# Kernel tuning notes

Measured on AMD Instinct MI355X. Metric: run time of the kernel, lower is better.

Reference implementation:

```python
import jax, jax.numpy as jnp
import numpy as np


def setup_inputs() -> dict:
    key = jax.random.key(0)
    ks = jax.random.split(key, 6)
    B, d, S = 256, 512, 196  # batch, hidden dim, spatial locations (14x14)
    return {
        "memory_state": jax.random.normal(ks[0], (B, d), dtype=jnp.float32),
        "ctrl_state": jax.random.normal(ks[1], (B, d), dtype=jnp.float32),
        "kb_proj": jax.random.normal(ks[2], (B, d, S), dtype=jnp.float32),
        "W_concat": jax.random.normal(ks[3], (d, d), dtype=jnp.float32) * (1.0 / np.sqrt(d)),
        "b_concat": jax.random.normal(ks[4], (d,), dtype=jnp.float32) * 0.01,
        "w_attn": jax.random.normal(ks[5], (d,), dtype=jnp.float32) * (1.0 / np.sqrt(d)),
    }


def reference(memory_state, ctrl_state, kb_proj, W_concat, b_concat, w_attn):
    # I_elements: [B, S, d] -- elementwise gating of knowledge base by memory
    I_t = memory_state[:, :, None] * kb_proj           # [B, d, S]
    I_t = jnp.transpose(I_t, (0, 2, 1))                # [B, S, d]
    # concat_layer (torch Linear: x @ W^T + b) + residual with kb_proj
    concat = jnp.einsum('bsd,ed->bse', I_t, W_concat) + b_concat
    concat = concat + jnp.transpose(kb_proj, (0, 2, 1))  # [B, S, d]
    # attention logits: (concat * ctrl) @ w_attn -> [B, S]
    rai = jnp.einsum('bsd,d->bs', concat * ctrl_state[:, None, :], w_attn)
    rvi = jax.nn.softmax(rai, axis=1)                  # [B, S]
    # attention-weighted sum over spatial locations -> [B, d]
    read_vector = jnp.einsum('bs,bds->bd', rvi, kb_proj)
    return read_vector
```

## Files before the change

### kernel.cpp

```cpp
#include <hip/hip_runtime.h>
#include <math.h>

#define B 256
#define D 512
#define S 196
#define SQ 49
#define NCH 8

__global__ __launch_bounds__(256) void k_gemm(const float* __restrict__ ctrl,
                                              const float* __restrict__ w_attn,
                                              const float* __restrict__ W,
                                              float* __restrict__ gpart) {
    __shared__ float u_s[64][8];
    const int ce = blockIdx.x >> 5;
    const int b0 = (blockIdx.x & 31) * 8;
    const int t = threadIdx.x;
#pragma unroll
    for (int k = t; k < 512; k += 256) {
        const int j = k & 7, el = k >> 3;
        const int e = ce * 64 + el;
        u_s[el][j] = ctrl[(b0 + j) * D + e] * w_attn[e];
    }
    __syncthreads();
    float a0[8], a1[8];
#pragma unroll
    for (int j = 0; j < 8; ++j) { a0[j] = 0.f; a1[j] = 0.f; }
    for (int e0 = 0; e0 < 64; e0 += 4) {
        float w0[4], w1[4];
#pragma unroll
        for (int i = 0; i < 4; ++i) {
            const int e = ce * 64 + e0 + i;
            w0[i] = W[e * D + t];
            w1[i] = W[e * D + t + 256];
        }
#pragma unroll
        for (int i = 0; i < 4; ++i) {
            const float4 ua = *(const float4*)&u_s[e0 + i][0];
            const float4 ub = *(const float4*)&u_s[e0 + i][4];
            a0[0] += ua.x * w0[i]; a0[1] += ua.y * w0[i];
            a0[2] += ua.z * w0[i]; a0[3] += ua.w * w0[i];
            a0[4] += ub.x * w0[i]; a0[5] += ub.y * w0[i];
            a0[6] += ub.z * w0[i]; a0[7] += ub.w * w0[i];
            a1[0] += ua.x * w1[i]; a1[1] += ua.y * w1[i];
            a1[2] += ua.z * w1[i]; a1[3] += ua.w * w1[i];
            a1[4] += ub.x * w1[i]; a1[5] += ub.y * w1[i];
            a1[6] += ub.z * w1[i]; a1[7] += ub.w * w1[i];
        }
    }
#pragma unroll
    for (int j = 0; j < 8; ++j) {
        gpart[((size_t)(b0 + j) * NCH + ce) * D + t]       = a0[j];
        gpart[((size_t)(b0 + j) * NCH + ce) * D + t + 256] = a1[j];
    }
}

__global__ __launch_bounds__(256) void k_logits(const float* __restrict__ kb,
                                                const float* __restrict__ gpart,
                                                const float* __restrict__ mem,
                                                const float* __restrict__ ctrl,
                                                const float* __restrict__ w_attn,
                                                float* __restrict__ rai_part) {
    __shared__ float p_s[64];
    __shared__ float part[4][S];
    const int bid = blockIdx.x;
    const int b = bid >> 3, c = bid & 7;
    const int t = threadIdx.x;
    const int w = t >> 6, l = t & 63;
    if (t < 64) {
        const int d = c * 64 + t;
        float s = 0.f;
#pragma unroll
        for (int ce = 0; ce < NCH; ++ce)
            s += gpart[((size_t)b * NCH + ce) * D + d];
        p_s[t] = mem[b * D + d] * s + ctrl[b * D + d] * w_attn[d];
    }
    __syncthreads();
    const float* base = kb + (size_t)b * D * S + (size_t)c * 64 * S;
    if (l < SQ) {
        float4 acc0 = {0.f, 0.f, 0.f, 0.f}, acc1 = {0.f, 0.f, 0.f, 0.f};
        for (int i = 0; i < 8; ++i) {
            const int r0 = w * 16 + i, r1 = w * 16 + 8 + i;
            const float4 v0 = *(const float4*)(base + (size_t)r0 * S + 4 * l);
            const float4 v1 = *(const float4*)(base + (size_t)r1 * S + 4 * l);
            const float pv0 = p_s[r0], pv1 = p_s[r1];
            acc0.x += pv0 * v0.x; acc0.y += pv0 * v0.y;
            acc0.z += pv0 * v0.z; acc0.w += pv0 * v0.w;
            acc1.x += pv1 * v1.x; acc1.y += pv1 * v1.y;
            acc1.z += pv1 * v1.z; acc1.w += pv1 * v1.w;
        }
        part[w][4 * l + 0] = acc0.x + acc1.x;
        part[w][4 * l + 1] = acc0.y + acc1.y;
        part[w][4 * l + 2] = acc0.z + acc1.z;
        part[w][4 * l + 3] = acc0.w + acc1.w;
    }
    __syncthreads();
    if (t < S)
        rai_part[(size_t)bid * S + t] = (part[0][t] + part[1][t]) + (part[2][t] + part[3][t]);
}

__global__ __launch_bounds__(256) void k_wsum(const float* __restrict__ kb,
                                              const float* __restrict__ rai_part,
                                              float* __restrict__ out) {
    __shared__ float rvi_s[S];
    __shared__ float redm[4], reds[4];
    const int bid = blockIdx.x;
    const int b = bid >> 3, c = bid & 7;
    const int t = threadIdx.x;
    const int w = t >> 6, l = t & 63;
    float rai = -INFINITY;
    if (t < S) {
        float v = 0.f;
#pragma unroll
        for (int k = 0; k < NCH; ++k)
            v += rai_part[((size_t)b * NCH + k) * S + t];
        rai = v;
    }
    float m = rai;
#pragma unroll
    for (int o = 1; o < 64; o <<= 1) m = fmaxf(m, __shfl_xor(m, o, 64));
    if (l == 0) redm[w] = m;
    __syncthreads();
    m = fmaxf(fmaxf(redm[0], redm[1]), fmaxf(redm[2], redm[3]));
    float ex = (t < S) ? __expf(rai - m) : 0.f;
    float sm = ex;
#pragma unroll
    for (int o = 1; o < 64; o <<= 1) sm += __shfl_xor(sm, o, 64);
    if (l == 0) reds[w] = sm;
    __syncthreads();
    const float li = (reds[0] + reds[1]) + (reds[2] + reds[3]);
    if (t < S) rvi_s[t] = ex / li;
    __syncthreads();

    float4 rv = {0.f, 0.f, 0.f, 0.f};
    if (l < SQ) rv = *(const float4*)&rvi_s[4 * l];
    const float* base = kb + (size_t)b * D * S + (size_t)c * 64 * S;
#pragma unroll
    for (int i = 0; i < 8; ++i) {
        const int r0 = w * 16 + i, r1 = w * 16 + 8 + i;
        float a0 = 0.f, a1 = 0.f;
        if (l < SQ) {
            const float4 v0 = *(const float4*)(base + (size_t)r0 * S + 4 * l);
            const float4 v1 = *(const float4*)(base + (size_t)r1 * S + 4 * l);
            a0 = rv.x * v0.x + rv.y * v0.y + rv.z * v0.z + rv.w * v0.w;
            a1 = rv.x * v1.x + rv.y * v1.y + rv.z * v1.z + rv.w * v1.w;
        }
#pragma unroll
        for (int o = 1; o < 64; o <<= 1) {
            a0 += __shfl_xor(a0, o, 64);
            a1 += __shfl_xor(a1, o, 64);
        }
        if (l == 0) {
            out[(size_t)b * D + c * 64 + r0] = a0;
            out[(size_t)b * D + c * 64 + r1] = a1;
        }
    }
}

extern "C" void kernel_launch(void* const* d_in, const int* in_sizes, int n_in,
                              void* d_out, int out_size, void* d_ws, size_t ws_size,
                              hipStream_t stream) {
    const float* mem  = (const float*)d_in[0];
    const float* ctrl = (const float*)d_in[1];
    const float* kb   = (const float*)d_in[2];
    const float* W    = (const float*)d_in[3];
    const float* wat  = (const float*)d_in[5];
    float* out = (float*)d_out;

    float* gpart    = (float*)d_ws;
    float* rai_part = gpart + (size_t)B * NCH * D;

    k_gemm  <<<256,     256, 0, stream>>>(ctrl, wat, W, gpart);
    k_logits<<<B * NCH, 256, 0, stream>>>(kb, gpart, mem, ctrl, wat, rai_part);
    k_wsum  <<<B * NCH, 256, 0, stream>>>(kb, rai_part, out);
}
```

Measured before the change: 189.6 us.

## Stage kb tiles into LDS with async global_load_lds in logits and wsum kernels

Both kb-reading kernels now issue direct global-to-LDS loads for their whole 64x196 kb tile at kernel start. The loads are in flight while the block computes p (logits) or the softmax (wsum), and the later dot products then read from shared memory. The aim is to hide global-load latency behind the prologue work and to issue wide, fully coalesced loads. In exchange, each block now holds about 50KB of LDS, which limits how many blocks fit per CU. Correctness also relies on the barrier waiting for the async LDS writes to finish.

```diff
diff --git a/kernel.cpp b/kernel.cpp
--- a/kernel.cpp
+++ b/kernel.cpp
@@ -6,6 +6,15 @@
 #define S 196
 #define SQ 49
 #define NCH 8
+#define NINST 49
+
+__device__ __forceinline__ void stage1k(const float* __restrict__ g,
+                                        float* lds_base, int lane) {
+    __builtin_amdgcn_global_load_lds(
+        (const __attribute__((address_space(1))) void*)(g + 4 * lane),
+        (__attribute__((address_space(3))) void*)lds_base,
+        16, 0, 0);
+}
 
 __global__ __launch_bounds__(256) void k_gemm(const float* __restrict__ ctrl,
                                               const float* __restrict__ w_attn,
@@ -60,12 +69,18 @@
                                                 const float* __restrict__ ctrl,
                                                 const float* __restrict__ w_attn,
                                                 float* __restrict__ rai_part) {
+    __shared__ float kb_s[64 * S];
     __shared__ float p_s[64];
     __shared__ float part[4][S];
     const int bid = blockIdx.x;
     const int b = bid >> 3, c = bid & 7;
     const int t = threadIdx.x;
     const int w = t >> 6, l = t & 63;
+    const float* base = kb + (size_t)b * D * S + (size_t)c * 64 * S;
+
+    for (int inst = w; inst < NINST; inst += 4)
+        stage1k(base + inst * 256, &kb_s[inst * 256], l);
+
     if (t < 64) {
         const int d = c * 64 + t;
         float s = 0.f;
@@ -75,23 +90,18 @@
         p_s[t] = mem[b * D + d] * s + ctrl[b * D + d] * w_attn[d];
     }
     __syncthreads();
-    const float* base = kb + (size_t)b * D * S + (size_t)c * 64 * S;
+
     if (l < SQ) {
-        float4 acc0 = {0.f, 0.f, 0.f, 0.f}, acc1 = {0.f, 0.f, 0.f, 0.f};
-        for (int i = 0; i < 8; ++i) {
-            const int r0 = w * 16 + i, r1 = w * 16 + 8 + i;
-            const float4 v0 = *(const float4*)(base + (size_t)r0 * S + 4 * l);
-            const float4 v1 = *(const float4*)(base + (size_t)r1 * S + 4 * l);
-            const float pv0 = p_s[r0], pv1 = p_s[r1];
-            acc0.x += pv0 * v0.x; acc0.y += pv0 * v0.y;
-            acc0.z += pv0 * v0.z; acc0.w += pv0 * v0.w;
-            acc1.x += pv1 * v1.x; acc1.y += pv1 * v1.y;
-            acc1.z += pv1 * v1.z; acc1.w += pv1 * v1.w;
+        float4 acc = {0.f, 0.f, 0.f, 0.f};
+#pragma unroll
+        for (int i = 0; i < 16; ++i) {
+            const int r = w * 16 + i;
+            const float4 v = *(const float4*)&kb_s[r * S + 4 * l];
+            const float pv = p_s[r];
+            acc.x += pv * v.x; acc.y += pv * v.y;
+            acc.z += pv * v.z; acc.w += pv * v.w;
         }
-        part[w][4 * l + 0] = acc0.x + acc1.x;
-        part[w][4 * l + 1] = acc0.y + acc1.y;
-        part[w][4 * l + 2] = acc0.z + acc1.z;
-        part[w][4 * l + 3] = acc0.w + acc1.w;
+        *(float4*)&part[w][4 * l] = acc;
     }
     __syncthreads();
     if (t < S)
@@ -101,12 +111,18 @@
 __global__ __launch_bounds__(256) void k_wsum(const float* __restrict__ kb,
                                               const float* __restrict__ rai_part,
                                               float* __restrict__ out) {
+    __shared__ float kb_s[64 * S];
     __shared__ float rvi_s[S];
     __shared__ float redm[4], reds[4];
     const int bid = blockIdx.x;
     const int b = bid >> 3, c = bid & 7;
     const int t = threadIdx.x;
     const int w = t >> 6, l = t & 63;
+    const float* base = kb + (size_t)b * D * S + (size_t)c * 64 * S;
+
+    for (int inst = w; inst < NINST; inst += 4)
+        stage1k(base + inst * 256, &kb_s[inst * 256], l);
+
     float rai = -INFINITY;
     if (t < S) {
         float v = 0.f;
@@ -133,26 +149,17 @@
 
     float4 rv = {0.f, 0.f, 0.f, 0.f};
     if (l < SQ) rv = *(const float4*)&rvi_s[4 * l];
-    const float* base = kb + (size_t)b * D * S + (size_t)c * 64 * S;
 #pragma unroll
-    for (int i = 0; i < 8; ++i) {
-        const int r0 = w * 16 + i, r1 = w * 16 + 8 + i;
-        float a0 = 0.f, a1 = 0.f;
+    for (int i = 0; i < 16; ++i) {
+        const int r = w * 16 + i;
+        float a = 0.f;
         if (l < SQ) {
-            const float4 v0 = *(const float4*)(base + (size_t)r0 * S + 4 * l);
-            const float4 v1 = *(const float4*)(base + (size_t)r1 * S + 4 * l);
-            a0 = rv.x * v0.x + rv.y * v0.y + rv.z * v0.z + rv.w * v0.w;
-            a1 = rv.x * v1.x + rv.y * v1.y + rv.z * v1.z + rv.w * v1.w;
+            const float4 v = *(const float4*)&kb_s[r * S + 4 * l];
+            a = rv.x * v.x + rv.y * v.y + rv.z * v.z + rv.w * v.w;
         }
 #pragma unroll
-        for (int o = 1; o < 64; o <<= 1) {
-            a0 += __shfl_xor(a0, o, 64);
-            a1 += __shfl_xor(a1, o, 64);
-        }
-        if (l == 0) {
-            out[(size_t)b * D + c * 64 + r0] = a0;
-            out[(size_t)b * D + c * 64 + r1] = a1;
-        }
+        for (int o = 1; o < 64; o <<= 1) a += __shfl_xor(a, o, 64);
+        if (l == 0) out[(size_t)b * D + c * 64 + r] = a;
     }
 }
 
```

Result: slower. 198.0 us (+4.5%).
